# Kernel tuning notes

Measured on AMD Instinct MI355X. Metric: run time of the kernel, lower is better.

The kernel has to match this reference:

```python
import jax, jax.numpy as jnp
import numpy as np

DIM, HEAD, R = 192, 8, 3
RR = 2 * R + 1
RA = RR * RR  # 49-sample local window


def conv2d(x, w, b):
    y = jax.lax.conv_general_dilated(x, w, (1, 1), 'SAME',
                                     dimension_numbers=('NCHW', 'OIHW', 'NCHW'))
    return y + b[None, :, None, None]


def _pix(c, size):
    # normalized [-1,1] -> pixel coord, align_corners=False
    return (c + 1.0) * (size * 0.5) - 0.5


def _gather(img, iy, ix, valid=None):
    # img [B,C,H,W]; iy/ix int [B,...] -> [B,C,...]; zero-fill where not valid
    B, C, H, W = img.shape
    sh = iy.shape
    idx = (jnp.clip(iy, 0, H - 1) * W + jnp.clip(ix, 0, W - 1)).reshape(B, -1)
    g = jax.vmap(lambda f, i: f[:, i])(img.reshape(B, C, H * W), idx)
    g = g.reshape((B, C) + sh[1:])
    if valid is not None:
        g = g * valid.reshape((B, 1) + sh[1:]).astype(g.dtype)
    return g


def bilinear_sample(img, cy, cx, border=False):
    # F.grid_sample bilinear, align_corners=False; cy/cx [B,Q] -> [B,C,Q]
    B, C, H, W = img.shape
    py, px = _pix(cy, H), _pix(cx, W)
    y0f, x0f = jnp.floor(py), jnp.floor(px)
    wy, wx = py - y0f, px - x0f
    y0, x0 = y0f.astype(jnp.int32), x0f.astype(jnp.int32)
    out = 0.0
    for dy, sy in ((0, 1.0 - wy), (1, wy)):
        for dx, sx in ((0, 1.0 - wx), (1, wx)):
            iy, ix = y0 + dy, x0 + dx
            valid = None if border else ((iy >= 0) & (iy < H) & (ix >= 0) & (ix < W))
            out = out + _gather(img, iy, ix, valid) * (sy * sx)[:, None]
    return out


def nearest_sample(img, cy, cx):
    # F.grid_sample nearest, align_corners=False, padding_mode='zeros'
    B, C, H, W = img.shape
    iy = jnp.floor(_pix(cy, H) + 0.5).astype(jnp.int32)
    ix = jnp.floor(_pix(cx, W) + 0.5).astype(jnp.int32)
    valid = (iy >= 0) & (iy < H) & (ix >= 0) & (ix < W)
    return _gather(img, iy, ix, valid)


def mlp(x, ws, bs):
    for w, b in zip(ws[:-1], bs[:-1]):
        x = jax.nn.relu(x @ w + b)
    return x @ ws[-1] + bs[-1]


def reference(inp, sample_coord, cell, enc_w, enc_b, ch_w, ch_b, q_w, q_b,
              k_w, k_b, v_w, v_b, m0w, m0b, m1w, m1b, m2w, m2b, m3w, m3b, m4w, m4b):
    # gen_feat: encoder (conv stand-in) -> conv_ch -> q/k/v convs
    feat = conv2d(conv2d(inp, enc_w, enc_b), ch_w, ch_b)
    feat_q = conv2d(feat, q_w, q_b)
    feat_k = conv2d(feat, k_w, k_b)
    feat_v = conv2d(feat, v_w, v_b)
    B, _, H, W = feat.shape
    Q = sample_coord.shape[1]
    hd = DIM // HEAD

    cy, cx = sample_coord[..., 0], sample_coord[..., 1]
    # sample_coord_k: nearest LR pixel-center coords (grid_sample nearest over make_coord grid)
    iy = jnp.clip(jnp.floor(_pix(cy, H) + 0.5), 0, H - 1)
    ix = jnp.clip(jnp.floor(_pix(cx, W) + 0.5), 0, W - 1)
    sky = -1.0 + (2.0 * iy + 1.0) / H
    skx = -1.0 + (2.0 * ix + 1.0) / W

    dh = jnp.linspace(-R, R, RR, dtype=jnp.float32) * (2.0 / H)
    dw = jnp.linspace(-R, R, RR, dtype=jnp.float32) * (2.0 / W)
    gy, gx = jnp.meshgrid(dh, dw, indexing='ij')
    cky = sky[..., None] + gy.reshape(-1)  # [B,Q,RA]
    ckx = skx[..., None] + gx.reshape(-1)

    q = bilinear_sample(feat_q, cy, cx)                       # [B,DIM,Q]
    q = q.transpose(0, 2, 1).reshape(B, Q, HEAD, hd)
    k = nearest_sample(feat_k, cky, ckx)                      # [B,DIM,Q,RA]
    k = k.transpose(0, 2, 3, 1).reshape(B, Q, RA, HEAD, hd)
    v = nearest_sample(feat_v, cky, ckx)
    v = v.transpose(0, 2, 3, 1).reshape(B, Q, RA, HEAD, hd)

    attn = jnp.einsum('bqhd,bqrhd->bqrh', q, k) / np.sqrt(hd).astype(np.float32)
    attn = jax.nn.softmax(attn, axis=2)                       # softmax over window
    v = (v * attn[..., None]).reshape(B, Q, RA * DIM)         # weighted, NOT summed

    rel_cell = cell[:, None, :] * jnp.array([H, W], jnp.float32)
    rel_cell = jnp.broadcast_to(rel_cell, (B, Q, 2))
    feat_in = jnp.concatenate([v, rel_cell], axis=-1)         # [B,Q,DIM*RA+2]

    pred = mlp(feat_in, [m0w, m1w, m2w, m3w, m4w], [m0b, m1b, m2b, m3b, m4b])
    base = bilinear_sample(inp, cy, cx, border=True).transpose(0, 2, 1)  # [B,Q,3]
    return pred + base


def setup_inputs() -> dict:
    key = jax.random.key(0)
    ks = jax.random.split(key, 16)
    B, H, W, Q = 2, 64, 64, 4096
    enc_out, hidden = 64, 256
    in_dim = DIM * RA + 2

    def cw(k, o, i):
        return jax.random.normal(k, (o, i, 3, 3), jnp.float32) / np.sqrt(i * 9.0)

    def lw(k, i, o):
        return jax.random.normal(k, (i, o), jnp.float32) / np.sqrt(float(i))

    return {
        'inp': jax.random.normal(ks[0], (B, 3, H, W), jnp.float32),
        'sample_coord': jax.random.uniform(ks[1], (B, Q, 2), jnp.float32, -1.0, 1.0),
        'cell': jnp.full((B, 2), 2.0 / 128.0, jnp.float32),
        'enc_w': cw(ks[2], enc_out, 3), 'enc_b': jnp.zeros((enc_out,), jnp.float32),
        'ch_w': cw(ks[3], DIM, enc_out), 'ch_b': jnp.zeros((DIM,), jnp.float32),
        'q_w': cw(ks[4], DIM, DIM), 'q_b': jnp.zeros((DIM,), jnp.float32),
        'k_w': cw(ks[5], DIM, DIM), 'k_b': jnp.zeros((DIM,), jnp.float32),
        'v_w': cw(ks[6], DIM, DIM), 'v_b': jnp.zeros((DIM,), jnp.float32),
        'm0w': lw(ks[7], in_dim, hidden), 'm0b': jnp.zeros((hidden,), jnp.float32),
        'm1w': lw(ks[8], hidden, hidden), 'm1b': jnp.zeros((hidden,), jnp.float32),
        'm2w': lw(ks[9], hidden, hidden), 'm2b': jnp.zeros((hidden,), jnp.float32),
        'm3w': lw(ks[10], hidden, hidden), 'm3b': jnp.zeros((hidden,), jnp.float32),
        'm4w': lw(ks[11], hidden, 3), 'm4b': jnp.zeros((3,), jnp.float32),
    }
```

## Files before the change

### kernel.cpp

```cpp
#include <hip/hip_runtime.h>
#include <hip/hip_bf16.h>


constexpr int BB = 2, QQ = 4096, DIMC = 192, RAW = 49;
constexpr int ENC = 64, P1 = 66, P3 = 70;

typedef __attribute__((ext_vector_type(8))) short bf16x8;
typedef __attribute__((ext_vector_type(8))) unsigned short u16x8;
typedef __attribute__((ext_vector_type(4))) float f32x4;

__device__ inline short f2bf(float f) {
  __hip_bfloat16 h = __float2bfloat16(f);
  return __builtin_bit_cast(short, h);
}
__device__ inline float bf2f(unsigned short u) {
  return __uint_as_float(((unsigned)u) << 16);
}

constexpr long long F_F1 = 0;
constexpr long long F_FEAT = 278784;
constexpr long long F_FQ = 1115136;
constexpr long long ZA_END = 2787840;
constexpr long long F_PART = 0;
constexpr long long F_FKB = 4194304;
constexpr long long F_FVB = 5135104;
constexpr long long F_ATTN = 6075904;
constexpr long long F_W0T = 7681536;
constexpr long long F_WTCH = 8885760;
constexpr long long F_WTQ = 8941056;
constexpr long long F_WTK = 9106944;
constexpr long long F_WTV = 9272832;
constexpr long long F_WFC1 = 9438720;
constexpr long long F_WFC2 = 9471488;
constexpr long long F_WFC3 = 9504256;
constexpr long long F_HA = 9537024;
constexpr long long F_HB = 10585600;

__global__ __launch_bounds__(256) void k_zero(float4* p, int n4) {
  int i = blockIdx.x * 256 + threadIdx.x;
  float4 z = make_float4(0.f, 0.f, 0.f, 0.f);
  for (; i < n4; i += gridDim.x * 256) p[i] = z;
}

__global__ __launch_bounds__(256) void k_w0t(const float* __restrict__ w0,
                                             short* __restrict__ w0t) {
  __shared__ short sh[64][72];
  int k0 = blockIdx.x * 64, n0 = blockIdx.y * 64;
  int t = threadIdx.x;
  #pragma unroll
  for (int i = 0; i < 16; i++) {
    int idx = t + i * 256;
    int r = idx >> 6, cc = idx & 63;
    sh[cc][r] = f2bf(w0[(long long)(k0 + r) * 256 + n0 + cc]);
  }
  __syncthreads();
  #pragma unroll
  for (int i = 0; i < 16; i++) {
    int idx = t + i * 256;
    int n = idx >> 6, k = idx & 63;
    w0t[(long long)(n0 + n) * 9408 + k0 + k] = sh[n][k];
  }
}

__global__ __launch_bounds__(256) void k_wtb(const float* __restrict__ w,
                                             short* __restrict__ wtb, int CI, int CO) {
  int g = blockIdx.x * 256 + threadIdx.x;
  if (g >= CO * CI * 9) return;
  int co = g / (CI * 9);
  int r = g - co * CI * 9;
  int ci = r / 9, t = r - ci * 9;
  wtb[(long long)co * (9 * CI) + t * CI + ci] = f2bf(w[g]);
}

__global__ __launch_bounds__(256) void k_wfc(const float* __restrict__ w,
                                             short* __restrict__ wt) {
  int n = blockIdx.x, k = threadIdx.x;
  wt[n * 256 + k] = f2bf(w[k * 256 + n]);
}

__global__ __launch_bounds__(256) void k_conv1(const float* __restrict__ inp,
                                               const float* __restrict__ ew,
                                               const float* __restrict__ eb,
                                               unsigned short* __restrict__ f1p) {
  int g = blockIdx.x * 256 + threadIdx.x;
  int co = g & 63, x = (g >> 6) & 63, y = (g >> 12) & 63, b = g >> 18;
  float acc = eb[co];
  #pragma unroll
  for (int ci = 0; ci < 3; ci++)
    #pragma unroll
    for (int ky = 0; ky < 3; ky++) {
      int yy = y + ky - 1;
      if (yy < 0 || yy > 63) continue;
      #pragma unroll
      for (int kx = 0; kx < 3; kx++) {
        int xx = x + kx - 1;
        if (xx < 0 || xx > 63) continue;
        acc += inp[((b * 3 + ci) * 64 + yy) * 64 + xx] * ew[((co * 3 + ci) * 3 + ky) * 3 + kx];
      }
    }
  f1p[((b * P1 + y + 1) * P1 + (x + 1)) * ENC + co] = (unsigned short)f2bf(acc);
}

template <int CIN, bool OF32>
__global__ __launch_bounds__(256) void k_conv3x3m(const unsigned short* __restrict__ in,
                                                  const short* __restrict__ wtb,
                                                  const float* __restrict__ bias,
                                                  void* __restrict__ outv, int pitchO,
                                                  int padO) {
  constexpr int NCH = CIN / 64;
  int nb = blockIdx.x;
  int by = blockIdx.y;
  int b = by >> 6, y = by & 63;
  int t = threadIdx.x;
  int lane = t & 63, w = t >> 6, wr = w >> 1, wc = w & 1;
  __shared__ __align__(16) short As[64][72];
  __shared__ __align__(16) short Bs[64][72];
  f32x4 acc[2][2];
  #pragma unroll
  for (int i = 0; i < 2; i++)
    #pragma unroll
    for (int j = 0; j < 2; j++) acc[i][j] = (f32x4){0.f, 0.f, 0.f, 0.f};
  int arow = t >> 2, kq4 = t & 3;
  int nbase = nb * 64;
  const long long K9 = 9LL * CIN;
  for (int c = 0; c < 9 * NCH; c++) {
    int t9 = c / NCH, sub = c - t9 * NCH;
    int dy = t9 / 3 - 1, dx = t9 % 3 - 1;
    __syncthreads();
    {
      const unsigned short* src = in +
          (((long long)b * P1 + y + dy + 1) * P1 + (arow + dx + 1)) * CIN + sub * 64 + kq4 * 16;
      *(bf16x8*)&As[arow][kq4 * 16] = *(const bf16x8*)src;
      *(bf16x8*)&As[arow][kq4 * 16 + 8] = *(const bf16x8*)(src + 8);
      const short* wp = wtb + (long long)(nbase + arow) * K9 + c * 64 + kq4 * 16;
      *(bf16x8*)&Bs[arow][kq4 * 16] = *(const bf16x8*)wp;
      *(bf16x8*)&Bs[arow][kq4 * 16 + 8] = *(const bf16x8*)(wp + 8);
    }
    __syncthreads();
    #pragma unroll
    for (int kk = 0; kk < 2; kk++) {
      bf16x8 a0 = *(const bf16x8*)&As[wr * 32 + (lane & 15)][kk * 32 + (lane >> 4) * 8];
      bf16x8 a1 = *(const bf16x8*)&As[wr * 32 + 16 + (lane & 15)][kk * 32 + (lane >> 4) * 8];
      bf16x8 b0 = *(const bf16x8*)&Bs[wc * 32 + (lane & 15)][kk * 32 + (lane >> 4) * 8];
      bf16x8 b1 = *(const bf16x8*)&Bs[wc * 32 + 16 + (lane & 15)][kk * 32 + (lane >> 4) * 8];
      acc[0][0] = __builtin_amdgcn_mfma_f32_16x16x32_bf16(a0, b0, acc[0][0], 0, 0, 0);
      acc[0][1] = __builtin_amdgcn_mfma_f32_16x16x32_bf16(a0, b1, acc[0][1], 0, 0, 0);
      acc[1][0] = __builtin_amdgcn_mfma_f32_16x16x32_bf16(a1, b0, acc[1][0], 0, 0, 0);
      acc[1][1] = __builtin_amdgcn_mfma_f32_16x16x32_bf16(a1, b1, acc[1][1], 0, 0, 0);
    }
  }
  int col0 = nbase + wc * 32 + (lane & 15);
  int row0 = wr * 32 + ((lane >> 4) << 2);
  #pragma unroll
  for (int nf = 0; nf < 2; nf++) {
    int co = col0 + nf * 16;
    float bv = bias[co];
    #pragma unroll
    for (int mf = 0; mf < 2; mf++)
      #pragma unroll
      for (int i = 0; i < 4; i++) {
        int x = row0 + mf * 16 + i;
        long long oi = (((long long)b * pitchO + y + padO) * pitchO + (x + padO)) * DIMC + co;
        float val = acc[mf][nf][i] + bv;
        if (OF32) ((float*)outv)[oi] = val;
        else ((unsigned short*)outv)[oi] = (unsigned short)f2bf(val);
      }
  }
}

__global__ __launch_bounds__(64) void k_attn(const float* __restrict__ sc,
                                             const float* __restrict__ fq,
                                             const unsigned short* __restrict__ fkb,
                                             unsigned short* __restrict__ attnO) {
  int bq = blockIdx.x;
  int b = bq >> 12;
  int lane = threadIdx.x;
  float cy = sc[bq * 2 + 0], cx = sc[bq * 2 + 1];
  float py = (cy + 1.f) * 32.f - 0.5f, px = (cx + 1.f) * 32.f - 0.5f;
  float fy = floorf(py), fx = floorf(px);
  float wy = py - fy, wx = px - fx;
  int iy = (int)fy, ix = (int)fx;
  __shared__ __align__(16) float qv[192];
  {
    const float* base = fq + (((long long)b * P1 + iy + 1) * P1 + (ix + 1)) * DIMC;
    #pragma unroll
    for (int u = 0; u < 3; u++) {
      int c = lane * 3 + u;
      float v00 = base[c], v01 = base[DIMC + c];
      float v10 = base[P1 * DIMC + c], v11 = base[P1 * DIMC + DIMC + c];
      qv[c] = (1.f - wy) * ((1.f - wx) * v00 + wx * v01) +
              wy * ((1.f - wx) * v10 + wx * v11);
    }
  }
  __syncthreads();
  int icy = min(max((int)floorf(py + 0.5f), 0), 63);
  int icx = min(max((int)floorf(px + 0.5f), 0), 63);
  float l[8];
  #pragma unroll
  for (int h = 0; h < 8; h++) l[h] = -1e30f;
  if (lane < 49) {
    int dy = lane / 7 - 3, dx = lane % 7 - 3;
    const unsigned short* kb =
        fkb + (((long long)b * P3 + icy + dy + 3) * P3 + (icx + dx + 3)) * DIMC;
    #pragma unroll
    for (int h = 0; h < 8; h++) l[h] = 0.f;
    #pragma unroll
    for (int c8 = 0; c8 < 24; c8++) {
      u16x8 k8 = *(const u16x8*)(kb + c8 * 8);
      float4 qa = *(const float4*)&qv[c8 * 8];
      float4 qb = *(const float4*)&qv[c8 * 8 + 4];
      l[c8 / 3] += qa.x * bf2f(k8[0]) + qa.y * bf2f(k8[1]) + qa.z * bf2f(k8[2]) +
                   qa.w * bf2f(k8[3]) + qb.x * bf2f(k8[4]) + qb.y * bf2f(k8[5]) +
                   qb.z * bf2f(k8[6]) + qb.w * bf2f(k8[7]);
    }
    const float s = 0.20412414523193154f;
    #pragma unroll
    for (int h = 0; h < 8; h++) l[h] *= s;
  }
  bf16x8 a8;
  #pragma unroll
  for (int h = 0; h < 8; h++) {
    float mx = l[h];
    #pragma unroll
    for (int s = 1; s < 64; s <<= 1) mx = fmaxf(mx, __shfl_xor(mx, s));
    float e = (lane < 49) ? expf(l[h] - mx) : 0.f;
    float sm = e;
    #pragma unroll
    for (int s = 1; s < 64; s <<= 1) sm += __shfl_xor(sm, s);
    a8[h] = f2bf(e / sm);
  }
  if (lane < 49) {
    *(bf16x8*)(attnO + ((long long)bq * 49 + lane) * 8) = a8;
  }
}

__global__ __launch_bounds__(256) void k_l0m(const float* __restrict__ sc,
                                             const unsigned short* __restrict__ fvb,
                                             const unsigned short* __restrict__ attn,
                                             const short* __restrict__ w0t,
                                             float* __restrict__ part) {
  int L = blockIdx.x + (blockIdx.y << 2);
  int xcd = L & 7, slot = L >> 3;
  int kq = xcd >> 2, nh = (xcd >> 1) & 1;
  int mb = ((xcd & 1) << 6) | slot;
  int qbase = mb * 64;
  int b = mb >> 6;
  int t = threadIdx.x;
  int lane = t & 63, w = t >> 6, wr = w >> 1, wc = w & 1;
  __shared__ __align__(16) short As[64][72];
  __shared__ __align__(16) short Bs[128][72];
  int arow = t >> 2, kq4 = t & 3;
  int q = qbase + arow;
  float cy = sc[q * 2 + 0], cx = sc[q * 2 + 1];
  float py = (cy + 1.f) * 32.f - 0.5f, px = (cx + 1.f) * 32.f - 0.5f;
  int icy = min(max((int)floorf(py + 0.5f), 0), 63);
  int icx = min(max((int)floorf(px + 0.5f), 0), 63);
  const unsigned short* fvp = fvb + (((long long)b * P3 + icy + 3) * P3 + (icx + 3)) * DIMC;
  const unsigned short* ap = attn + (long long)q * 392;
  int ch0 = kq4 * 16;
  int nbase = nh * 128;
  int nB = t >> 1, hB = t & 1;
  f32x4 acc[2][4];
  #pragma unroll
  for (int i = 0; i < 2; i++)
    #pragma unroll
    for (int j = 0; j < 4; j++) acc[i][j] = (f32x4){0.f, 0.f, 0.f, 0.f};
  int c0 = kq * 74, cnt = kq ? 73 : 74;
  for (int ci = 0; ci < cnt; ci++) {
    int cc = c0 + ci;
    int r = cc / 3, sub = cc - r * 3;
    int dy2 = r / 7 - 3, dx2 = r % 7 - 3;
    long long tap = ((long long)dy2 * P3 + dx2) * DIMC;
    __syncthreads();
    {
      const unsigned short* src = fvp + tap + sub * 64 + ch0;
      u16x8 r0 = *(const u16x8*)src;
      u16x8 r1 = *(const u16x8*)(src + 8);
      int cA = sub * 64 + ch0;
      float a0 = bf2f(ap[r * 8 + cA / 24]);
      float a1 = bf2f(ap[r * 8 + (cA + 8) / 24]);
      bf16x8 pk0, pk1;
      #pragma unroll
      for (int e = 0; e < 8; e++) pk0[e] = f2bf(bf2f(r0[e]) * a0);
      #pragma unroll
      for (int e = 0; e < 8; e++) pk1[e] = f2bf(bf2f(r1[e]) * a1);
      *(bf16x8*)&As[arow][ch0] = pk0;
      *(bf16x8*)&As[arow][ch0 + 8] = pk1;
      const short* wp = w0t + (long long)(nbase + nB) * 9408 + cc * 64 + hB * 32;
      *(bf16x8*)&Bs[nB][hB * 32] = *(const bf16x8*)wp;
      *(bf16x8*)&Bs[nB][hB * 32 + 8] = *(const bf16x8*)(wp + 8);
      *(bf16x8*)&Bs[nB][hB * 32 + 16] = *(const bf16x8*)(wp + 16);
      *(bf16x8*)&Bs[nB][hB * 32 + 24] = *(const bf16x8*)(wp + 24);
    }
    __syncthreads();
    #pragma unroll
    for (int kk = 0; kk < 2; kk++) {
      bf16x8 av[2], bv[4];
      #pragma unroll
      for (int mf = 0; mf < 2; mf++)
        av[mf] = *(const bf16x8*)&As[wr * 32 + mf * 16 + (lane & 15)][kk * 32 + (lane >> 4) * 8];
      #pragma unroll
      for (int nf = 0; nf < 4; nf++)
        bv[nf] = *(const bf16x8*)&Bs[wc * 64 + nf * 16 + (lane & 15)][kk * 32 + (lane >> 4) * 8];
      #pragma unroll
      for (int mf = 0; mf < 2; mf++)
        #pragma unroll
        for (int nf = 0; nf < 4; nf++)
          acc[mf][nf] = __builtin_amdgcn_mfma_f32_16x16x32_bf16(av[mf], bv[nf], acc[mf][nf], 0, 0, 0);
    }
  }
  float* p = part + (long long)kq * 2097152;
  int row0 = wr * 32 + ((lane >> 4) << 2);
  int col0 = nbase + wc * 64 + (lane & 15);
  #pragma unroll
  for (int mf = 0; mf < 2; mf++)
    #pragma unroll
    for (int nf = 0; nf < 4; nf++)
      #pragma unroll
      for (int i = 0; i < 4; i++)
        p[(long long)(qbase + row0 + mf * 16 + i) * 256 + col0 + nf * 16] = acc[mf][nf][i];
}

__global__ __launch_bounds__(256) void k_l0red(const float* __restrict__ part,
                                               const float* __restrict__ cell,
                                               const float* __restrict__ w0,
                                               const float* __restrict__ b0,
                                               unsigned short* __restrict__ h) {
  int gid = blockIdx.x * 256 + threadIdx.x;
  int q = gid >> 6, n0 = (gid & 63) << 2;
  int b = q >> 12;
  float rc0 = cell[b * 2 + 0] * 64.f, rc1 = cell[b * 2 + 1] * 64.f;
  float4 s0 = ((const float4*)part)[gid];
  float4 s1 = ((const float4*)(part + 2097152))[gid];
  unsigned short o[4];
  #pragma unroll
  for (int j = 0; j < 4; j++) {
    int n = n0 + j;
    float tailv = rc0 * w0[9408LL * 256 + n] + rc1 * w0[9409LL * 256 + n] + b0[n];
    float v = ((const float*)&s0)[j] + ((const float*)&s1)[j] + tailv;
    o[j] = (unsigned short)f2bf(fmaxf(v, 0.f));
  }
  *(uint2*)(h + (long long)gid * 4) = *(uint2*)o;
}

__global__ __launch_bounds__(256) void k_fcm(const unsigned short* __restrict__ hin,
                                             const short* __restrict__ wt,
                                             const float* __restrict__ bias,
                                             unsigned short* __restrict__ hout) {
  int nb = blockIdx.x, mb = blockIdx.y;
  int qbase = mb * 64, nbase = nb * 64;
  int t = threadIdx.x;
  int lane = t & 63, w = t >> 6, wr = w >> 1, wc = w & 1;
  __shared__ __align__(16) short As[64][264];
  __shared__ __align__(16) short Bs[64][264];
  int row = t >> 2, seg = t & 3;
  {
    const unsigned short* hp = hin + (long long)(qbase + row) * 256 + seg * 64;
    const short* wp = wt + (long long)(nbase + row) * 256 + seg * 64;
    #pragma unroll
    for (int j = 0; j < 8; j++) {
      *(bf16x8*)&As[row][seg * 64 + j * 8] = *(const bf16x8*)(hp + j * 8);
      *(bf16x8*)&Bs[row][seg * 64 + j * 8] = *(const bf16x8*)(wp + j * 8);
    }
  }
  __syncthreads();
  f32x4 acc[2][2];
  #pragma unroll
  for (int i = 0; i < 2; i++)
    #pragma unroll
    for (int j = 0; j < 2; j++) acc[i][j] = (f32x4){0.f, 0.f, 0.f, 0.f};
  #pragma unroll
  for (int kk = 0; kk < 8; kk++) {
    bf16x8 a0 = *(const bf16x8*)&As[wr * 32 + (lane & 15)][kk * 32 + (lane >> 4) * 8];
    bf16x8 a1 = *(const bf16x8*)&As[wr * 32 + 16 + (lane & 15)][kk * 32 + (lane >> 4) * 8];
    bf16x8 b0 = *(const bf16x8*)&Bs[wc * 32 + (lane & 15)][kk * 32 + (lane >> 4) * 8];
    bf16x8 b1 = *(const bf16x8*)&Bs[wc * 32 + 16 + (lane & 15)][kk * 32 + (lane >> 4) * 8];
    acc[0][0] = __builtin_amdgcn_mfma_f32_16x16x32_bf16(a0, b0, acc[0][0], 0, 0, 0);
    acc[0][1] = __builtin_amdgcn_mfma_f32_16x16x32_bf16(a0, b1, acc[0][1], 0, 0, 0);
    acc[1][0] = __builtin_amdgcn_mfma_f32_16x16x32_bf16(a1, b0, acc[1][0], 0, 0, 0);
    acc[1][1] = __builtin_amdgcn_mfma_f32_16x16x32_bf16(a1, b1, acc[1][1], 0, 0, 0);
  }
  int row0 = wr * 32 + ((lane >> 4) << 2);
  int col0 = nbase + wc * 32 + (lane & 15);
  #pragma unroll
  for (int nf = 0; nf < 2; nf++) {
    int n = col0 + nf * 16;
    float bv = bias[n];
    #pragma unroll
    for (int mf = 0; mf < 2; mf++)
      #pragma unroll
      for (int i = 0; i < 4; i++)
        hout[(long long)(qbase + row0 + mf * 16 + i) * 256 + n] =
            (unsigned short)f2bf(fmaxf(acc[mf][nf][i] + bv, 0.f));
  }
}

__global__ __launch_bounds__(64) void k_final(const unsigned short* __restrict__ h3,
                                              const float* __restrict__ w4,
                                              const float* __restrict__ b4,
                                              const float* __restrict__ sc,
                                              const float* __restrict__ inp,
                                              float* __restrict__ out) {
  int bq = blockIdx.x;
  int b = bq >> 12;
  int lane = threadIdx.x;
  float p0 = 0.f, p1 = 0.f, p2 = 0.f;
  const unsigned short* hr = h3 + (long long)bq * 256;
  #pragma unroll
  for (int u = 0; u < 4; u++) {
    int c = lane + u * 64;
    float hv = bf2f(hr[c]);
    p0 += hv * w4[c * 3 + 0];
    p1 += hv * w4[c * 3 + 1];
    p2 += hv * w4[c * 3 + 2];
  }
  #pragma unroll
  for (int s = 1; s < 64; s <<= 1) {
    p0 += __shfl_xor(p0, s);
    p1 += __shfl_xor(p1, s);
    p2 += __shfl_xor(p2, s);
  }
  if (lane == 0) {
    float cy = sc[bq * 2 + 0], cx = sc[bq * 2 + 1];
    float py = (cy + 1.f) * 32.f - 0.5f, px = (cx + 1.f) * 32.f - 0.5f;
    float fy = floorf(py), fx = floorf(px);
    float wy = py - fy, wx = px - fx;
    int y0 = (int)fy, x0 = (int)fx;
    int yc0 = min(max(y0, 0), 63), yc1 = min(max(y0 + 1, 0), 63);
    int xc0 = min(max(x0, 0), 63), xc1 = min(max(x0 + 1, 0), 63);
    float o[3] = {p0 + b4[0], p1 + b4[1], p2 + b4[2]};
    #pragma unroll
    for (int j = 0; j < 3; j++) {
      const float* im = inp + ((long long)b * 3 + j) * 4096;
      float s00 = im[yc0 * 64 + xc0], s01 = im[yc0 * 64 + xc1];
      float s10 = im[yc1 * 64 + xc0], s11 = im[yc1 * 64 + xc1];
      o[j] += (1.f - wy) * ((1.f - wx) * s00 + wx * s01) +
              wy * ((1.f - wx) * s10 + wx * s11);
      out[(long long)bq * 3 + j] = o[j];
    }
  }
}

extern "C" void kernel_launch(void* const* d_in, const int* in_sizes, int n_in,
                              void* d_out, int out_size, void* d_ws, size_t ws_size,
                              hipStream_t stream) {
  const float* inp = (const float*)d_in[0];
  const float* sc = (const float*)d_in[1];
  const float* cell = (const float*)d_in[2];
  const float* enc_w = (const float*)d_in[3];
  const float* enc_b = (const float*)d_in[4];
  const float* ch_w = (const float*)d_in[5];
  const float* ch_b = (const float*)d_in[6];
  const float* q_w = (const float*)d_in[7];
  const float* q_b = (const float*)d_in[8];
  const float* k_w = (const float*)d_in[9];
  const float* k_b = (const float*)d_in[10];
  const float* v_w = (const float*)d_in[11];
  const float* v_b = (const float*)d_in[12];
  const float* m0w = (const float*)d_in[13];
  const float* m0b = (const float*)d_in[14];
  const float* m1w = (const float*)d_in[15];
  const float* m1b = (const float*)d_in[16];
  const float* m2w = (const float*)d_in[17];
  const float* m2b = (const float*)d_in[18];
  const float* m3w = (const float*)d_in[19];
  const float* m3b = (const float*)d_in[20];
  const float* m4w = (const float*)d_in[21];
  const float* m4b = (const float*)d_in[22];
  float* ws = (float*)d_ws;
  unsigned short* f1p = (unsigned short*)(ws + F_F1);
  unsigned short* featp = (unsigned short*)(ws + F_FEAT);
  float* featqp = ws + F_FQ;
  float* part = ws + F_PART;
  unsigned short* fkb = (unsigned short*)(ws + F_FKB);
  unsigned short* fvb = (unsigned short*)(ws + F_FVB);
  unsigned short* attnb = (unsigned short*)(ws + F_ATTN);
  short* w0t = (short*)(ws + F_W0T);
  short* wtb_ch = (short*)(ws + F_WTCH);
  short* wtb_q = (short*)(ws + F_WTQ);
  short* wtb_k = (short*)(ws + F_WTK);
  short* wtb_v = (short*)(ws + F_WTV);
  short* wfc1 = (short*)(ws + F_WFC1);
  short* wfc2 = (short*)(ws + F_WFC2);
  short* wfc3 = (short*)(ws + F_WFC3);
  unsigned short* h_a = (unsigned short*)(ws + F_HA);
  unsigned short* h_b = (unsigned short*)(ws + F_HB);
  float* outp = (float*)d_out;

  k_zero<<<1024, 256, 0, stream>>>((float4*)ws, (int)(ZA_END / 4));
  k_zero<<<1024, 256, 0, stream>>>((float4*)(ws + F_FKB), (int)(1881600 / 4));
  k_w0t<<<dim3(147, 4), 256, 0, stream>>>(m0w, w0t);
  k_wtb<<<(192 * 64 * 9 + 255) / 256, 256, 0, stream>>>(ch_w, wtb_ch, 64, 192);
  k_wtb<<<(192 * 192 * 9 + 255) / 256, 256, 0, stream>>>(q_w, wtb_q, 192, 192);
  k_wtb<<<(192 * 192 * 9 + 255) / 256, 256, 0, stream>>>(k_w, wtb_k, 192, 192);
  k_wtb<<<(192 * 192 * 9 + 255) / 256, 256, 0, stream>>>(v_w, wtb_v, 192, 192);
  k_wfc<<<256, 256, 0, stream>>>(m1w, wfc1);
  k_wfc<<<256, 256, 0, stream>>>(m2w, wfc2);
  k_wfc<<<256, 256, 0, stream>>>(m3w, wfc3);
  k_conv1<<<(BB * 64 * 64 * ENC) / 256, 256, 0, stream>>>(inp, enc_w, enc_b, f1p);
  k_conv3x3m<64, false><<<dim3(3, BB * 64), 256, 0, stream>>>(f1p, wtb_ch, ch_b, featp, P1, 1);
  k_conv3x3m<192, true><<<dim3(3, BB * 64), 256, 0, stream>>>(featp, wtb_q, q_b, featqp, P1, 1);
  k_conv3x3m<192, false><<<dim3(3, BB * 64), 256, 0, stream>>>(featp, wtb_k, k_b, fkb, P3, 3);
  k_conv3x3m<192, false><<<dim3(3, BB * 64), 256, 0, stream>>>(featp, wtb_v, v_b, fvb, P3, 3);
  k_attn<<<BB * QQ, 64, 0, stream>>>(sc, featqp, fkb, attnb);
  k_l0m<<<dim3(4, 128), 256, 0, stream>>>(sc, fvb, attnb, w0t, part);
  k_l0red<<<2048, 256, 0, stream>>>(part, cell, m0w, m0b, h_a);
  k_fcm<<<dim3(4, 128), 256, 0, stream>>>(h_a, wfc1, m1b, h_b);
  k_fcm<<<dim3(4, 128), 256, 0, stream>>>(h_b, wfc2, m2b, h_a);
  k_fcm<<<dim3(4, 128), 256, 0, stream>>>(h_a, wfc3, m3b, h_b);
  k_final<<<BB * QQ, 64, 0, stream>>>(h_b, m4w, m4b, sc, inp, outp);
}
```

Before: 386.1 us.

## Fuse weight-prep launches and split layer-0 GEMM K eight ways with atomics

Merges the zeroing kernels into one launch and the eight weight-transpose launches into one prep kernel, cutting launch overhead. The layer-0 GEMM now gives each block a full 256-wide N tile and splits K into eight chunks instead of two. Partial results are accumulated with float atomicAdd into a zeroed buffer, which removes the second partial sum from the reduction. The cost is atomic traffic, a larger shared B tile, twice as many accumulator registers, and dropping the XCD-aware block remapping.

```diff
diff --git a/kernel.cpp b/kernel.cpp
--- a/kernel.cpp
+++ b/kernel.cpp
@@ -21,7 +21,6 @@
 constexpr long long F_FEAT = 278784;
 constexpr long long F_FQ = 1115136;
 constexpr long long ZA_END = 2787840;
-constexpr long long F_PART = 0;
 constexpr long long F_FKB = 4194304;
 constexpr long long F_FVB = 5135104;
 constexpr long long F_ATTN = 6075904;
@@ -35,47 +34,72 @@
 constexpr long long F_WFC3 = 9504256;
 constexpr long long F_HA = 9537024;
 constexpr long long F_HB = 10585600;
-
-__global__ __launch_bounds__(256) void k_zero(float4* p, int n4) {
-  int i = blockIdx.x * 256 + threadIdx.x;
+constexpr long long F_PART = 11634176;
+
+__global__ __launch_bounds__(256) void k_zero3(float4* ws4) {
+  const int a4 = (int)(ZA_END / 4);
+  const int b4 = 470400;
+  const int c4 = 524288;
+  int n4 = a4 + b4 + c4;
   float4 z = make_float4(0.f, 0.f, 0.f, 0.f);
-  for (; i < n4; i += gridDim.x * 256) p[i] = z;
-}
-
-__global__ __launch_bounds__(256) void k_w0t(const float* __restrict__ w0,
-                                             short* __restrict__ w0t) {
+  for (int i = blockIdx.x * 256 + threadIdx.x; i < n4; i += gridDim.x * 256) {
+    float4* p;
+    if (i < a4) p = ws4 + i;
+    else if (i < a4 + b4) p = ws4 + (int)(F_FKB / 4) + (i - a4);
+    else p = ws4 + (int)(F_PART / 4) + (i - a4 - b4);
+    *p = z;
+  }
+}
+
+__global__ __launch_bounds__(256) void k_prep(
+    const float* __restrict__ m0w, const float* __restrict__ ch_w,
+    const float* __restrict__ q_w, const float* __restrict__ k_w,
+    const float* __restrict__ v_w, const float* __restrict__ m1w,
+    const float* __restrict__ m2w, const float* __restrict__ m3w,
+    short* __restrict__ w0t, short* __restrict__ wtb_ch, short* __restrict__ wtb_q,
+    short* __restrict__ wtb_k, short* __restrict__ wtb_v, short* __restrict__ wfc1,
+    short* __restrict__ wfc2, short* __restrict__ wfc3) {
   __shared__ short sh[64][72];
-  int k0 = blockIdx.x * 64, n0 = blockIdx.y * 64;
-  int t = threadIdx.x;
-  #pragma unroll
-  for (int i = 0; i < 16; i++) {
-    int idx = t + i * 256;
-    int r = idx >> 6, cc = idx & 63;
-    sh[cc][r] = f2bf(w0[(long long)(k0 + r) * 256 + n0 + cc]);
-  }
-  __syncthreads();
-  #pragma unroll
-  for (int i = 0; i < 16; i++) {
-    int idx = t + i * 256;
-    int n = idx >> 6, k = idx & 63;
-    w0t[(long long)(n0 + n) * 9408 + k0 + k] = sh[n][k];
-  }
-}
-
-__global__ __launch_bounds__(256) void k_wtb(const float* __restrict__ w,
-                                             short* __restrict__ wtb, int CI, int CO) {
-  int g = blockIdx.x * 256 + threadIdx.x;
-  if (g >= CO * CI * 9) return;
-  int co = g / (CI * 9);
-  int r = g - co * CI * 9;
-  int ci = r / 9, t = r - ci * 9;
-  wtb[(long long)co * (9 * CI) + t * CI + ci] = f2bf(w[g]);
-}
-
-__global__ __launch_bounds__(256) void k_wfc(const float* __restrict__ w,
-                                             short* __restrict__ wt) {
-  int n = blockIdx.x, k = threadIdx.x;
-  wt[n * 256 + k] = f2bf(w[k * 256 + n]);
+  int bb = blockIdx.x, t = threadIdx.x;
+  if (bb < 588) {
+    int k0 = (bb % 147) * 64, n0 = (bb / 147) * 64;
+    #pragma unroll
+    for (int i = 0; i < 16; i++) {
+      int idx = t + i * 256;
+      int r = idx >> 6, cc = idx & 63;
+      sh[cc][r] = f2bf(m0w[(long long)(k0 + r) * 256 + n0 + cc]);
+    }
+    __syncthreads();
+    #pragma unroll
+    for (int i = 0; i < 16; i++) {
+      int idx = t + i * 256;
+      int n = idx >> 6, k = idx & 63;
+      w0t[(long long)(n0 + n) * 9408 + k0 + k] = sh[n][k];
+    }
+    return;
+  }
+  const float* src = nullptr;
+  short* dst = nullptr;
+  int CI = 0, base = 0;
+  if (bb < 1020) { src = ch_w; dst = wtb_ch; CI = 64; base = 588; }
+  else if (bb < 2316) { src = q_w; dst = wtb_q; CI = 192; base = 1020; }
+  else if (bb < 3612) { src = k_w; dst = wtb_k; CI = 192; base = 2316; }
+  else if (bb < 4908) { src = v_w; dst = wtb_v; CI = 192; base = 3612; }
+  if (dst) {
+    int g = (bb - base) * 256 + t;
+    if (g < 192 * CI * 9) {
+      int co = g / (CI * 9);
+      int r = g - co * CI * 9;
+      int ci = r / 9, tp = r - ci * 9;
+      dst[(long long)co * (9 * CI) + tp * CI + ci] = f2bf(src[g]);
+    }
+    return;
+  }
+  const float* fsrc; short* fdst; int n;
+  if (bb < 5164) { fsrc = m1w; fdst = wfc1; n = bb - 4908; }
+  else if (bb < 5420) { fsrc = m2w; fdst = wfc2; n = bb - 5164; }
+  else { fsrc = m3w; fdst = wfc3; n = bb - 5420; }
+  fdst[n * 256 + t] = f2bf(fsrc[t * 256 + n]);
 }
 
 __global__ __launch_bounds__(256) void k_conv1(const float* __restrict__ inp,
@@ -239,16 +263,14 @@
                                              const unsigned short* __restrict__ attn,
                                              const short* __restrict__ w0t,
                                              float* __restrict__ part) {
-  int L = blockIdx.x + (blockIdx.y << 2);
-  int xcd = L & 7, slot = L >> 3;
-  int kq = xcd >> 2, nh = (xcd >> 1) & 1;
-  int mb = ((xcd & 1) << 6) | slot;
+  int kq = blockIdx.x;
+  int mb = blockIdx.y;
   int qbase = mb * 64;
   int b = mb >> 6;
   int t = threadIdx.x;
   int lane = t & 63, w = t >> 6, wr = w >> 1, wc = w & 1;
   __shared__ __align__(16) short As[64][72];
-  __shared__ __align__(16) short Bs[128][72];
+  __shared__ __align__(16) short Bs[256][72];
   int arow = t >> 2, kq4 = t & 3;
   int q = qbase + arow;
   float cy = sc[q * 2 + 0], cx = sc[q * 2 + 1];
@@ -258,14 +280,13 @@
   const unsigned short* fvp = fvb + (((long long)b * P3 + icy + 3) * P3 + (icx + 3)) * DIMC;
   const unsigned short* ap = attn + (long long)q * 392;
   int ch0 = kq4 * 16;
-  int nbase = nh * 128;
-  int nB = t >> 1, hB = t & 1;
-  f32x4 acc[2][4];
+  f32x4 acc[2][8];
   #pragma unroll
   for (int i = 0; i < 2; i++)
     #pragma unroll
-    for (int j = 0; j < 4; j++) acc[i][j] = (f32x4){0.f, 0.f, 0.f, 0.f};
-  int c0 = kq * 74, cnt = kq ? 73 : 74;
+    for (int j = 0; j < 8; j++) acc[i][j] = (f32x4){0.f, 0.f, 0.f, 0.f};
+  int c0 = kq * 18 + min(kq, 3);
+  int cnt = 18 + (kq < 3 ? 1 : 0);
   for (int ci = 0; ci < cnt; ci++) {
     int cc = c0 + ci;
     int r = cc / 3, sub = cc - r * 3;
@@ -286,39 +307,34 @@
       for (int e = 0; e < 8; e++) pk1[e] = f2bf(bf2f(r1[e]) * a1);
       *(bf16x8*)&As[arow][ch0] = pk0;
       *(bf16x8*)&As[arow][ch0 + 8] = pk1;
-      const short* wp = w0t + (long long)(nbase + nB) * 9408 + cc * 64 + hB * 32;
-      *(bf16x8*)&Bs[nB][hB * 32] = *(const bf16x8*)wp;
-      *(bf16x8*)&Bs[nB][hB * 32 + 8] = *(const bf16x8*)(wp + 8);
-      *(bf16x8*)&Bs[nB][hB * 32 + 16] = *(const bf16x8*)(wp + 16);
-      *(bf16x8*)&Bs[nB][hB * 32 + 24] = *(const bf16x8*)(wp + 24);
+      const short* wp = w0t + (long long)t * 9408 + cc * 64;
+      #pragma unroll
+      for (int j = 0; j < 8; j++)
+        *(bf16x8*)&Bs[t][j * 8] = *(const bf16x8*)(wp + j * 8);
     }
     __syncthreads();
     #pragma unroll
     for (int kk = 0; kk < 2; kk++) {
-      bf16x8 av[2], bv[4];
-      #pragma unroll
-      for (int mf = 0; mf < 2; mf++)
-        av[mf] = *(const bf16x8*)&As[wr * 32 + mf * 16 + (lane & 15)][kk * 32 + (lane >> 4) * 8];
-      #pragma unroll
-      for (int nf = 0; nf < 4; nf++)
-        bv[nf] = *(const bf16x8*)&Bs[wc * 64 + nf * 16 + (lane & 15)][kk * 32 + (lane >> 4) * 8];
-      #pragma unroll
-      for (int mf = 0; mf < 2; mf++)
-        #pragma unroll
-        for (int nf = 0; nf < 4; nf++)
-          acc[mf][nf] = __builtin_amdgcn_mfma_f32_16x16x32_bf16(av[mf], bv[nf], acc[mf][nf], 0, 0, 0);
-    }
-  }
-  float* p = part + (long long)kq * 2097152;
+      bf16x8 av0 = *(const bf16x8*)&As[wr * 32 + (lane & 15)][kk * 32 + (lane >> 4) * 8];
+      bf16x8 av1 = *(const bf16x8*)&As[wr * 32 + 16 + (lane & 15)][kk * 32 + (lane >> 4) * 8];
+      #pragma unroll
+      for (int nf = 0; nf < 8; nf++) {
+        bf16x8 bv = *(const bf16x8*)&Bs[wc * 128 + nf * 16 + (lane & 15)][kk * 32 + (lane >> 4) * 8];
+        acc[0][nf] = __builtin_amdgcn_mfma_f32_16x16x32_bf16(av0, bv, acc[0][nf], 0, 0, 0);
+        acc[1][nf] = __builtin_amdgcn_mfma_f32_16x16x32_bf16(av1, bv, acc[1][nf], 0, 0, 0);
+      }
+    }
+  }
   int row0 = wr * 32 + ((lane >> 4) << 2);
-  int col0 = nbase + wc * 64 + (lane & 15);
+  int colb = wc * 128 + (lane & 15);
   #pragma unroll
   for (int mf = 0; mf < 2; mf++)
     #pragma unroll
-    for (int nf = 0; nf < 4; nf++)
+    for (int nf = 0; nf < 8; nf++)
       #pragma unroll
       for (int i = 0; i < 4; i++)
-        p[(long long)(qbase + row0 + mf * 16 + i) * 256 + col0 + nf * 16] = acc[mf][nf][i];
+        atomicAdd(&part[(long long)(qbase + row0 + mf * 16 + i) * 256 + colb + nf * 16],
+                  acc[mf][nf][i]);
 }
 
 __global__ __launch_bounds__(256) void k_l0red(const float* __restrict__ part,
@@ -331,13 +347,12 @@
   int b = q >> 12;
   float rc0 = cell[b * 2 + 0] * 64.f, rc1 = cell[b * 2 + 1] * 64.f;
   float4 s0 = ((const float4*)part)[gid];
-  float4 s1 = ((const float4*)(part + 2097152))[gid];
   unsigned short o[4];
   #pragma unroll
   for (int j = 0; j < 4; j++) {
     int n = n0 + j;
     float tailv = rc0 * w0[9408LL * 256 + n] + rc1 * w0[9409LL * 256 + n] + b0[n];
-    float v = ((const float*)&s0)[j] + ((const float*)&s1)[j] + tailv;
+    float v = ((const float*)&s0)[j] + tailv;
     o[j] = (unsigned short)f2bf(fmaxf(v, 0.f));
   }
   *(uint2*)(h + (long long)gid * 4) = *(uint2*)o;
@@ -471,7 +486,6 @@
   unsigned short* f1p = (unsigned short*)(ws + F_F1);
   unsigned short* featp = (unsigned short*)(ws + F_FEAT);
   float* featqp = ws + F_FQ;
-  float* part = ws + F_PART;
   unsigned short* fkb = (unsigned short*)(ws + F_FKB);
   unsigned short* fvb = (unsigned short*)(ws + F_FVB);
   unsigned short* attnb = (unsigned short*)(ws + F_ATTN);
@@ -485,25 +499,19 @@
   short* wfc3 = (short*)(ws + F_WFC3);
   unsigned short* h_a = (unsigned short*)(ws + F_HA);
   unsigned short* h_b = (unsigned short*)(ws + F_HB);
+  float* part = ws + F_PART;
   float* outp = (float*)d_out;
 
-  k_zero<<<1024, 256, 0, stream>>>((float4*)ws, (int)(ZA_END / 4));
-  k_zero<<<1024, 256, 0, stream>>>((float4*)(ws + F_FKB), (int)(1881600 / 4));
-  k_w0t<<<dim3(147, 4), 256, 0, stream>>>(m0w, w0t);
-  k_wtb<<<(192 * 64 * 9 + 255) / 256, 256, 0, stream>>>(ch_w, wtb_ch, 64, 192);
-  k_wtb<<<(192 * 192 * 9 + 255) / 256, 256, 0, stream>>>(q_w, wtb_q, 192, 192);
-  k_wtb<<<(192 * 192 * 9 + 255) / 256, 256, 0, stream>>>(k_w, wtb_k, 192, 192);
-  k_wtb<<<(192 * 192 * 9 + 255) / 256, 256, 0, stream>>>(v_w, wtb_v, 192, 192);
-  k_wfc<<<256, 256, 0, stream>>>(m1w, wfc1);
-  k_wfc<<<256, 256, 0, stream>>>(m2w, wfc2);
-  k_wfc<<<256, 256, 0, stream>>>(m3w, wfc3);
+  k_zero3<<<2048, 256, 0, stream>>>((float4*)ws);
+  k_prep<<<5676, 256, 0, stream>>>(m0w, ch_w, q_w, k_w, v_w, m1w, m2w, m3w, w0t,
+                                   wtb_ch, wtb_q, wtb_k, wtb_v, wfc1, wfc2, wfc3);
   k_conv1<<<(BB * 64 * 64 * ENC) / 256, 256, 0, stream>>>(inp, enc_w, enc_b, f1p);
   k_conv3x3m<64, false><<<dim3(3, BB * 64), 256, 0, stream>>>(f1p, wtb_ch, ch_b, featp, P1, 1);
   k_conv3x3m<192, true><<<dim3(3, BB * 64), 256, 0, stream>>>(featp, wtb_q, q_b, featqp, P1, 1);
   k_conv3x3m<192, false><<<dim3(3, BB * 64), 256, 0, stream>>>(featp, wtb_k, k_b, fkb, P3, 3);
   k_conv3x3m<192, false><<<dim3(3, BB * 64), 256, 0, stream>>>(featp, wtb_v, v_b, fvb, P3, 3);
   k_attn<<<BB * QQ, 64, 0, stream>>>(sc, featqp, fkb, attnb);
-  k_l0m<<<dim3(4, 128), 256, 0, stream>>>(sc, fvb, attnb, w0t, part);
+  k_l0m<<<dim3(8, 128), 256, 0, stream>>>(sc, fvb, attnb, w0t, part);
   k_l0red<<<2048, 256, 0, stream>>>(part, cell, m0w, m0b, h_a);
   k_fcm<<<dim3(4, 128), 256, 0, stream>>>(h_a, wfc1, m1b, h_b);
   k_fcm<<<dim3(4, 128), 256, 0, stream>>>(h_b, wfc2, m2b, h_a);
```

Result: slower. 458.0 us (+18.6%).
